# Optimization experiments

Measured on AMD Instinct MI355X. Metric: run time of the kernel, lower is better.

Reference implementation:

```python
import jax, jax.numpy as jnp
import numpy as np
from jax import lax

DN = ('NCHW', 'OIHW', 'NCHW')

def _conv(x, w, b):
    # stride-2 conv, kernel 4, padding 1 (PyTorch Conv2d semantics)
    y = lax.conv_general_dilated(x, w, (2, 2), [(1, 1), (1, 1)], dimension_numbers=DN)
    return y + b[None, :, None, None]

def _deconv(x, w, b):
    # PyTorch ConvTranspose2d(k=4, stride=2, padding=1): conv with lhs_dilation=2,
    # padding k-1-p=2, kernel rot180 with in/out axes swapped ([I,O,H,W] -> [O,I,H,W])
    k = jnp.transpose(jnp.flip(w, (2, 3)), (1, 0, 2, 3))
    y = lax.conv_general_dilated(x, k, (1, 1), [(2, 2), (2, 2)], lhs_dilation=(2, 2),
                                 dimension_numbers=DN)
    return y + b[None, :, None, None]

def setup_inputs() -> dict:
    key = jax.random.key(0)
    ks = jax.random.split(key, 16)
    K, D = 1024, 2048
    s = lambda *sh: 0.05
    inp = {
        'x': jax.random.uniform(ks[0], (8, 3, 256, 256), jnp.float32),
        'enc_w1': jax.random.normal(ks[1], (128, 3, 4, 4), jnp.float32) * 0.05,
        'enc_b1': jnp.zeros((128,), jnp.float32),
        'enc_w2': jax.random.normal(ks[2], (128, 128, 4, 4), jnp.float32) * 0.02,
        'enc_b2': jnp.zeros((128,), jnp.float32),
        'enc_w3': jax.random.normal(ks[3], (D, 128, 4, 4), jnp.float32) * 0.02,
        'enc_b3': jnp.zeros((D,), jnp.float32),
        'codebook': jax.random.uniform(ks[4], (K, D), jnp.float32, -1.0 / K, 1.0 / K),
        'dec_w1': jax.random.normal(ks[5], (D, 128, 4, 4), jnp.float32) * 0.02,  # [in,out,kH,kW]
        'dec_b1': jnp.zeros((128,), jnp.float32),
        'dec_w2': jax.random.normal(ks[6], (128, 128, 4, 4), jnp.float32) * 0.02,
        'dec_b2': jnp.zeros((128,), jnp.float32),
        'dec_w3': jax.random.normal(ks[7], (128, 1, 4, 4), jnp.float32) * 0.05,
        'dec_b3': jnp.zeros((1,), jnp.float32),
    }
    return inp

def reference(x, enc_w1, enc_b1, enc_w2, enc_b2, enc_w3, enc_b3, codebook,
              dec_w1, dec_b1, dec_w2, dec_b2, dec_w3, dec_b3):
    # encoder
    h = jax.nn.relu(_conv(x, enc_w1, enc_b1))
    h = jax.nn.relu(_conv(h, enc_w2, enc_b2))
    z_e = _conv(h, enc_w3, enc_b3)                       # [B, D, H8, W8]
    B, D, Hq, Wq = z_e.shape
    z_flat = z_e.reshape(B, D, Hq * Wq).transpose(0, 2, 1)  # [B, N, D]
    # squared distances to codebook [K, D]
    dists = (jnp.sum(z_flat ** 2, axis=2, keepdims=True)
             + jnp.sum(codebook ** 2, axis=1)
             - 2.0 * jnp.einsum('bnd,kd->bnk', z_flat, codebook))  # [B, N, K]
    idx = jnp.argmin(dists, axis=2)                      # [B, N]
    z_q = codebook[idx]                                  # [B, N, D]
    z_q = z_q.transpose(0, 2, 1).reshape(B, D, Hq, Wq)
    # decoder
    h = jax.nn.relu(_deconv(z_q, dec_w1, dec_b1))
    h = jax.nn.relu(_deconv(h, dec_w2, dec_b2))
    x_recon = jax.nn.sigmoid(_deconv(h, dec_w3, dec_b3))  # [B, 1, H, W]
    sg = lax.stop_gradient
    commitment = 0.25 * jnp.mean((sg(z_e) - z_q) ** 2)
    quantization = jnp.mean((z_e - sg(z_q)) ** 2)
    return x_recon, commitment + quantization
```

## Files before the change

### kernel.cpp

```cpp
#include <hip/hip_runtime.h>

typedef __attribute__((ext_vector_type(8))) short bf16x8;
typedef __attribute__((ext_vector_type(4))) float f32x4;

__device__ __forceinline__ unsigned short f2bf(float f) {
  unsigned u = __float_as_uint(f);
  u += 0x7fff + ((u >> 16) & 1);
  return (unsigned short)(u >> 16);
}
__device__ __forceinline__ float bf2f(unsigned short h) {
  return __uint_as_float(((unsigned)h) << 16);
}

__device__ __forceinline__ void gload_lds16(const void* g, void* l) {
  __builtin_amdgcn_global_load_lds((const __attribute__((address_space(1))) void*)g,
                                   (__attribute__((address_space(3))) void*)l, 16, 0, 0);
}

__device__ __forceinline__ void pbar() {
  asm volatile("" ::: "memory");
  __builtin_amdgcn_sched_barrier(0);
  __builtin_amdgcn_s_barrier();
  __builtin_amdgcn_sched_barrier(0);
  asm volatile("" ::: "memory");
}

__global__ __launch_bounds__(256) void halo_k(unsigned short* __restrict__ h1,
                                              unsigned short* __restrict__ h2,
                                              unsigned short* __restrict__ h3,
                                              unsigned short* __restrict__ h4) {
  int pid = blockIdx.x * 2 + (threadIdx.x >> 7);
  int co = threadIdx.x & 127;
  unsigned short* buf;
  int b, e, SP;
  if (pid < 8256) {
    buf = (pid < 4128) ? h1 : h4;
    int rel = (pid < 4128) ? pid : pid - 4128;
    b = rel / 516; e = rel % 516; SP = 130;
    int y, x;
    if (e < 130) { y = 0; x = e; }
    else if (e < 260) { y = 129; x = e - 130; }
    else if (e < 388) { y = 1 + (e - 260); x = 0; }
    else { y = 1 + (e - 388); x = 129; }
    buf[(((size_t)(b * SP + y)) * SP + x) * 128 + co] = 0;
  } else {
    buf = (pid < 10336) ? h2 : h3;
    int rel = pid - ((pid < 10336) ? 8256 : 10336);
    b = rel / 260; e = rel % 260; SP = 66;
    int y, x;
    if (e < 66) { y = 0; x = e; }
    else if (e < 132) { y = 65; x = e - 66; }
    else if (e < 196) { y = 1 + (e - 132); x = 0; }
    else { y = 1 + (e - 196); x = 65; }
    buf[(((size_t)(b * SP + y)) * SP + x) * 128 + co] = 0;
  }
}

__global__ __launch_bounds__(256) void megapack_k(
    const float* __restrict__ ew2, const float* __restrict__ ew3,
    const float* __restrict__ dw1, const float* __restrict__ dw2,
    const float* __restrict__ dw3, unsigned short* __restrict__ bt2,
    unsigned short* __restrict__ bt3, unsigned short* __restrict__ btw1,
    unsigned short* __restrict__ btd2, float* __restrict__ wd3) {
  int i = blockIdx.x * 256 + threadIdx.x;
  if (i < 262144) {
    int ci = i & 127, kk = (i >> 7) & 15, co = i >> 11;
    bt2[i] = f2bf(ew2[(size_t)co * 2048 + ci * 16 + kk]);
  } else if (i < 4456448) {
    int j = i - 262144;
    int ci = j & 127, kk = (j >> 7) & 15, co = j >> 11;
    bt3[j] = f2bf(ew3[(size_t)co * 2048 + ci * 16 + kk]);
  } else if (i < 8650752) {
    int j = i - 4456448;
    int ci = j & 2047, n = j >> 11;
    int co = n & 127, t = n >> 7;
    btw1[j] = f2bf(dw1[(((size_t)ci * 128 + co) << 4) + t]);
  } else if (i < 8912896) {
    int j = i - 8650752;
    int ci = j & 127, t = (j >> 7) & 3, co = (j >> 9) & 127, z = j >> 16;
    int py = z >> 1, px = z & 1, ty = t >> 1, tx = t & 1;
    int ky = 2 * ty + 1 - py, kx = 2 * tx + 1 - px;
    btd2[j] = f2bf(dw2[(((size_t)ci * 128 + co) * 4 + ky) * 4 + kx]);
  } else {
    int j = i - 8912896;
    int ci = j & 127, t = (j >> 7) & 3, z = j >> 9;
    int py = z >> 1, px = z & 1, ty = t >> 1, tx = t & 1;
    int ky = 2 * ty + 1 - py, kx = 2 * tx + 1 - px;
    wd3[j] = dw3[ci * 16 + ky * 4 + kx];
  }
}

__global__ __launch_bounds__(256) void pack_cb(const float* __restrict__ cb,
                                               unsigned short* __restrict__ cbb,
                                               float* __restrict__ cnorm) {
  int r = blockIdx.x;
  const float* src = cb + (size_t)r * 2048;
  float s = 0.f;
  for (int i = threadIdx.x; i < 2048; i += 256) {
    float v = src[i];
    cbb[(size_t)r * 2048 + i] = f2bf(v);
    s += v * v;
  }
  __shared__ float red[4];
  for (int off = 32; off > 0; off >>= 1) s += __shfl_down(s, off, 64);
  int lane = threadIdx.x & 63, wid = threadIdx.x >> 6;
  if (lane == 0) red[wid] = s;
  __syncthreads();
  if (threadIdx.x == 0) cnorm[r] = red[0] + red[1] + red[2] + red[3];
}

__global__ __launch_bounds__(256) void conv1_k(const float* __restrict__ x,
                                               const float* __restrict__ w1,
                                               const float* __restrict__ b1,
                                               unsigned short* __restrict__ h1) {
  __shared__ float sIn[3][4][258];
  int b = blockIdx.x >> 7, y = blockIdx.x & 127;
  for (int i = threadIdx.x; i < 3 * 4 * 258; i += 256) {
    int c = i / (4 * 258);
    int rr = (i / 258) % 4;
    int col = i % 258;
    int iy = 2 * y - 1 + rr;
    int ix = col - 1;
    float v = (iy >= 0 && iy < 256 && ix >= 0 && ix < 256)
                  ? x[((size_t)(b * 3 + c) * 256 + iy) * 256 + ix] : 0.f;
    sIn[c][rr][col] = v;
  }
  __syncthreads();
  int co = threadIdx.x & 127, xh = threadIdx.x >> 7;
  float w[3][4][4];
#pragma unroll
  for (int c = 0; c < 3; ++c)
#pragma unroll
    for (int ky = 0; ky < 4; ++ky)
#pragma unroll
      for (int kx = 0; kx < 4; ++kx)
        w[c][ky][kx] = w1[(((size_t)co * 3 + c) * 4 + ky) * 4 + kx];
  float bb = b1[co];
  for (int xi = 0; xi < 64; ++xi) {
    int xx = xh * 64 + xi;
    float acc = bb;
#pragma unroll
    for (int c = 0; c < 3; ++c)
#pragma unroll
      for (int ky = 0; ky < 4; ++ky)
#pragma unroll
        for (int kx = 0; kx < 4; ++kx)
          acc += sIn[c][ky][2 * xx + kx] * w[c][ky][kx];
    acc = acc > 0.f ? acc : 0.f;
    h1[((size_t)(b * 130 + y + 1) * 130 + (xx + 1)) * 128 + co] = f2bf(acc);
  }
}

#define GM_CONV 0
#define GM_DECONV 1
#define GM_FLAT 2
#define EP_PM 0
#define EP_FLATBF 1
#define EP_F32 2

struct GP {
  const unsigned short* A;
  const unsigned short* Bt;
  const float* bias;
  void* out;
  int Klen, Clog;
  int MXlog, MYlog;
  int WPin, strideBA;
  int HPo, WPo;
  int Nout;
  int BrowStride;
  int BclassStride;
  int classLog;
  int TPC;
  int outZ;
};

template <int BM, int GM, int EP, int RELU>
__global__ __launch_bounds__(256) void gemm_k(GP p) {
  constexpr int MFR = BM / 32;
  constexpr int CA = BM / 32;
  const int tid = threadIdx.x;
  const int lane = tid & 63;
  const int wid = tid >> 6;
  const int m0 = blockIdx.x * BM;
  const int n0 = blockIdx.y * 128;
  const int zAll = blockIdx.z;
  const int zc = zAll & ((1 << p.classLog) - 1);
  const int chunk = zAll >> p.classLog;
  const int py = zc >> 1, px = zc & 1;

  __shared__ __align__(16) unsigned short sA[BM * 64];
  __shared__ __align__(16) unsigned short sB[128 * 64];

  const unsigned short* Bt = p.Bt + (size_t)zc * p.BclassStride;
  const int C = 1 << p.Clog;
  const int tb = chunk * p.TPC;
  const int chunkOff = tb << p.Clog;
  const int sw = ((lane & 7) ^ (lane >> 3)) * 8;

  int rcA[CA];
#pragma unroll
  for (int i = 0; i < CA; ++i) {
    int r = (wid * CA + i) * 8 + (lane >> 3);
    int m = m0 + r;
    if (GM == GM_FLAT) {
      rcA[i] = m * p.Klen;
    } else {
      int mx = m & ((1 << p.MXlog) - 1);
      int my = (m >> p.MXlog) & ((1 << p.MYlog) - 1);
      int b = m >> (p.MXlog + p.MYlog);
      if (GM == GM_CONV)
        rcA[i] = b * p.strideBA + ((2 * my) * p.WPin + 2 * mx) * C;
      else
        rcA[i] = b * p.strideBA + ((my + 1) * p.WPin + (mx + 1)) * C;
    }
  }
  int rcB[4];
#pragma unroll
  for (int i = 0; i < 4; ++i) {
    int r = (wid * 4 + i) * 8 + (lane >> 3);
    rcB[i] = (n0 + r) * p.BrowStride;
  }

  f32x4 acc[MFR][4];
#pragma unroll
  for (int a = 0; a < MFR; ++a)
#pragma unroll
    for (int b = 0; b < 4; ++b) acc[a][b] = (f32x4){0.f, 0.f, 0.f, 0.f};

  const int nsteps = p.Klen >> 6;
  for (int ks = 0; ks < nsteps; ++ks) {
    const int k0 = ks << 6;
    int tap = 0;
    if (GM == GM_CONV) {
      int t = tb + (k0 >> p.Clog);
      tap = ((t >> 2) * p.WPin + (t & 3)) * C;
    } else if (GM == GM_DECONV) {
      int t = tb + (k0 >> p.Clog);
      int ty = t >> 1, tx = t & 1;
      tap = ((py - ty) * p.WPin + (px - tx)) * C;
    }
    const int ci0 = k0 & (C - 1);
    const int aoff = tap + ci0 + sw;
#pragma unroll
    for (int i = 0; i < CA; ++i)
      gload_lds16(p.A + rcA[i] + aoff, &sA[(wid * CA + i) * 512]);
#pragma unroll
    for (int i = 0; i < 4; ++i)
      gload_lds16(Bt + rcB[i] + chunkOff + k0 + sw, &sB[(wid * 4 + i) * 512]);
    __syncthreads();

#pragma unroll
    for (int kk = 0; kk < 2; ++kk) {
      bf16x8 af[MFR], bfv[4];
#pragma unroll
      for (int mf = 0; mf < MFR; ++mf) {
        int row = (wid >> 1) * (BM / 2) + mf * 16 + (lane & 15);
        int col = (kk * 64 + ((lane >> 4) << 4)) ^ ((row & 7) << 4);
        af[mf] = *(const bf16x8*)((const char*)sA + row * 128 + col);
      }
#pragma unroll
      for (int nf = 0; nf < 4; ++nf) {
        int row = (wid & 1) * 64 + nf * 16 + (lane & 15);
        int col = (kk * 64 + ((lane >> 4) << 4)) ^ ((row & 7) << 4);
        bfv[nf] = *(const bf16x8*)((const char*)sB + row * 128 + col);
      }
#pragma unroll
      for (int mf = 0; mf < MFR; ++mf)
#pragma unroll
        for (int nf = 0; nf < 4; ++nf)
          acc[mf][nf] = __builtin_amdgcn_mfma_f32_16x16x32_bf16(
              af[mf], bfv[nf], acc[mf][nf], 0, 0, 0);
    }
    __syncthreads();
  }

  const int wr = wid >> 1, wc = wid & 1;
#pragma unroll
  for (int mf = 0; mf < MFR; ++mf) {
#pragma unroll
    for (int j = 0; j < 4; ++j) {
      int row = m0 + wr * (BM / 2) + mf * 16 + ((lane >> 4) << 2) + j;
      int b = 0, my = 0, mx = 0;
      if (EP == EP_PM) {
        mx = row & ((1 << p.MXlog) - 1);
        my = (row >> p.MXlog) & ((1 << p.MYlog) - 1);
        b = row >> (p.MXlog + p.MYlog);
      }
#pragma unroll
      for (int nf = 0; nf < 4; ++nf) {
        int col = n0 + wc * 64 + nf * 16 + (lane & 15);
        float v = acc[mf][nf][j];
        if (EP == EP_PM || EP == EP_FLATBF) v += p.bias[col];
        if (RELU) v = v > 0.f ? v : 0.f;
        if (EP == EP_F32) {
          ((float*)p.out)[(size_t)row * p.Nout + col] = v;
        } else if (EP == EP_FLATBF) {
          ((unsigned short*)p.out)[(size_t)row * p.Nout + col] = f2bf(v);
        } else {
          int oy, ox;
          if (GM == GM_DECONV) {
            oy = 2 * my + py + 1;
            ox = 2 * mx + px + 1;
          } else {
            oy = my + 1;
            ox = mx + 1;
          }
          ((unsigned short*)p.out)[((size_t)(b * p.HPo + oy) * p.WPo + ox) * 128 + col] =
              f2bf(v);
        }
      }
    }
  }
}

struct G2 {
  const unsigned short* A;
  const unsigned short* Bt;
  const float* bias;
  unsigned short* out;
  int Klen;
  int WPin, strideBA;
  int Nout;
};

template <int GM>
__global__ __launch_bounds__(512, 2) void gemm256_k(G2 p) {
  __shared__ __align__(16) unsigned short lds[8 * 8192];
  const int tid = threadIdx.x, lane = tid & 63, wid = tid >> 6;
  const int wr = wid >> 2, wc = wid & 3;
  const int m0 = blockIdx.x * 256, n0 = blockIdx.y * 256;
  const int sw = ((lane & 7) ^ (lane >> 3)) * 8;
  const int xc0 = ((lane >> 4) ^ (lane & 7)) * 16;
  const int xc1 = (((lane >> 4) | 4) ^ (lane & 7)) * 16;

  int rcA[2][2], rcB[2][2];
#pragma unroll
  for (int h = 0; h < 2; ++h)
#pragma unroll
    for (int i = 0; i < 2; ++i) {
      int m = m0 + h * 128 + wid * 16 + i * 8 + (lane >> 3);
      if (GM == GM_CONV) {
        int mx = m & 31, my = (m >> 5) & 31, b = m >> 10;
        rcA[h][i] = b * p.strideBA + ((2 * my) * p.WPin + 2 * mx) * 128;
      } else {
        rcA[h][i] = m * p.Klen;
      }
      int n = n0 + h * 128 + wid * 16 + i * 8 + (lane >> 3);
      rcB[h][i] = n * p.Klen;
    }

  const int JMAX = p.Klen >> 4;

  auto stage = [&](int j) {
    if (j >= JMAX) return;
    const int T = j >> 2, type = j & 3, slot = j & 7;
    unsigned short* dst = &lds[slot * 8192 + wid * 1024];
    if (type < 2) {
      const int ko = (T << 6) + sw;
      gload_lds16(p.Bt + rcB[type][0] + ko, dst);
      gload_lds16(p.Bt + rcB[type][1] + ko, dst + 512);
    } else {
      int ko;
      if (GM == GM_CONV) {
        const int t = T >> 1;
        ko = ((t >> 2) * p.WPin + (t & 3)) * 128 + ((T & 1) << 6) + sw;
      } else {
        ko = (T << 6) + sw;
      }
      gload_lds16(p.A + rcA[type - 2][0] + ko, dst);
      gload_lds16(p.A + rcA[type - 2][1] + ko, dst + 512);
    }
  };

  f32x4 acc[8][4];
#pragma unroll
  for (int i = 0; i < 8; ++i)
#pragma unroll
    for (int j = 0; j < 4; ++j) acc[i][j] = (f32x4){0.f, 0.f, 0.f, 0.f};

#pragma unroll
  for (int j = 0; j < 7; ++j) stage(j);
  asm volatile("s_waitcnt vmcnt(6)" ::: "memory");
  pbar();

  const int NT = p.Klen >> 6;
  bf16x8 a[4][2], b0[2][2], b1[2][2];
  for (int t = 0; t < NT; ++t) {
    const int sb = (t & 1) << 2;
    const char* myA = (const char*)&lds[(sb + 2 + wr) * 8192];
    const char* myB = (const char*)&lds[(sb + (wc >> 1)) * 8192];
    const int p4 = t << 2;
#pragma unroll
    for (int mf = 0; mf < 4; ++mf) {
      const int r = mf * 16 + (lane & 15);
      a[mf][0] = *(const bf16x8*)(myA + r * 128 + xc0);
      a[mf][1] = *(const bf16x8*)(myA + r * 128 + xc1);
    }
#pragma unroll
    for (int nf = 0; nf < 2; ++nf) {
      const int c = (wc & 1) * 64 + nf * 16 + (lane & 15);
      b0[nf][0] = *(const bf16x8*)(myB + c * 128 + xc0);
      b0[nf][1] = *(const bf16x8*)(myB + c * 128 + xc1);
    }
    stage(p4 + 7);
    pbar();
    __builtin_amdgcn_s_setprio(1);
#pragma unroll
    for (int mf = 0; mf < 4; ++mf)
#pragma unroll
      for (int nf = 0; nf < 2; ++nf)
#pragma unroll
        for (int kk = 0; kk < 2; ++kk)
          acc[mf][nf] = __builtin_amdgcn_mfma_f32_16x16x32_bf16(
              a[mf][kk], b0[nf][kk], acc[mf][nf], 0, 0, 0);
    __builtin_amdgcn_s_setprio(0);
    pbar();
#pragma unroll
    for (int nf = 0; nf < 2; ++nf) {
      const int c = (wc & 1) * 64 + (nf + 2) * 16 + (lane & 15);
      b1[nf][0] = *(const bf16x8*)(myB + c * 128 + xc0);
      b1[nf][1] = *(const bf16x8*)(myB + c * 128 + xc1);
    }
    stage(p4 + 8);
    pbar();
    __builtin_amdgcn_s_setprio(1);
#pragma unroll
    for (int mf = 0; mf < 4; ++mf)
#pragma unroll
      for (int nf = 0; nf < 2; ++nf)
#pragma unroll
        for (int kk = 0; kk < 2; ++kk)
          acc[mf][nf + 2] = __builtin_amdgcn_mfma_f32_16x16x32_bf16(
              a[mf][kk], b1[nf][kk], acc[mf][nf + 2], 0, 0, 0);
    __builtin_amdgcn_s_setprio(0);
    pbar();
#pragma unroll
    for (int mf = 0; mf < 4; ++mf) {
      const int r = 64 + mf * 16 + (lane & 15);
      a[mf][0] = *(const bf16x8*)(myA + r * 128 + xc0);
      a[mf][1] = *(const bf16x8*)(myA + r * 128 + xc1);
    }
    stage(p4 + 9);
    pbar();
    __builtin_amdgcn_s_setprio(1);
#pragma unroll
    for (int mf = 0; mf < 4; ++mf)
#pragma unroll
      for (int nf = 0; nf < 2; ++nf)
#pragma unroll
        for (int kk = 0; kk < 2; ++kk)
          acc[mf + 4][nf + 2] = __builtin_amdgcn_mfma_f32_16x16x32_bf16(
              a[mf][kk], b1[nf][kk], acc[mf + 4][nf + 2], 0, 0, 0);
    __builtin_amdgcn_s_setprio(0);
    pbar();
    stage(p4 + 10);
    pbar();
    __builtin_amdgcn_s_setprio(1);
#pragma unroll
    for (int mf = 0; mf < 4; ++mf)
#pragma unroll
      for (int nf = 0; nf < 2; ++nf)
#pragma unroll
        for (int kk = 0; kk < 2; ++kk)
          acc[mf + 4][nf] = __builtin_amdgcn_mfma_f32_16x16x32_bf16(
              a[mf][kk], b0[nf][kk], acc[mf + 4][nf], 0, 0, 0);
    __builtin_amdgcn_s_setprio(0);
    asm volatile("s_waitcnt vmcnt(6)" ::: "memory");
    pbar();
  }

#pragma unroll
  for (int mf = 0; mf < 8; ++mf) {
#pragma unroll
    for (int j = 0; j < 4; ++j) {
      int row = m0 + wr * 128 + mf * 16 + ((lane >> 4) << 2) + j;
#pragma unroll
      for (int nf = 0; nf < 4; ++nf) {
        int col = n0 + wc * 64 + nf * 16 + (lane & 15);
        float v = acc[mf][nf][j] + p.bias[col];
        p.out[(size_t)row * p.Nout + col] = f2bf(v);
      }
    }
  }
}

struct GV {
  const unsigned short* A;
  const unsigned short* Bt;
  const float* cnorm;
  float* cval;
  int* cidx;
};

__global__ __launch_bounds__(512, 2) void vq8_k(GV p) {
  __shared__ __align__(16) unsigned short lds[49152];
  const int tid = threadIdx.x, lane = tid & 63, wid = tid >> 6;
  const int wr = wid >> 2, wc = wid & 3;
  const int m0 = blockIdx.x * 128, n0 = blockIdx.y * 256;
  const int sw = ((lane & 7) ^ (lane >> 3)) * 8;
  const int xc0 = ((lane >> 4) ^ (lane & 7)) * 16;
  const int xc1 = (((lane >> 4) | 4) ^ (lane & 7)) * 16;
  const int K = 2048;

  int rcA[2];
#pragma unroll
  for (int h = 0; h < 2; ++h)
    rcA[h] = (m0 + h * 64 + wid * 8 + (lane >> 3)) * K;
  int rcB[2][2];
#pragma unroll
  for (int h = 0; h < 2; ++h)
#pragma unroll
    for (int i = 0; i < 2; ++i)
      rcB[h][i] = (n0 + h * 128 + wid * 16 + i * 8 + (lane >> 3)) * K;

  auto stage = [&](int j) {
    if (j >= 128) return;
    const int T = j >> 2, type = j & 3;
    unsigned short* reg = &lds[(T & 1) * 24576];
    const int ko = (T << 6) + sw;
    if (type < 2) {
      gload_lds16(p.A + rcA[type] + ko, reg + type * 4096 + wid * 512);
    } else {
      unsigned short* d = reg + 8192 + (type - 2) * 8192 + wid * 1024;
      gload_lds16(p.Bt + rcB[type - 2][0] + ko, d);
      gload_lds16(p.Bt + rcB[type - 2][1] + ko, d + 512);
    }
  };

  f32x4 acc[4][4];
#pragma unroll
  for (int i = 0; i < 4; ++i)
#pragma unroll
    for (int j = 0; j < 4; ++j) acc[i][j] = (f32x4){0.f, 0.f, 0.f, 0.f};

#pragma unroll
  for (int j = 0; j < 6; ++j) stage(j);
  asm volatile("s_waitcnt vmcnt(2)" ::: "memory");
  pbar();

  bf16x8 a[4][2], b[4][2];
  for (int t = 0; t < 32; ++t) {
    const char* reg = (const char*)&lds[(t & 1) * 24576];
    const char* myA = reg + wr * 8192;
    const char* myB = reg + 16384 + (wc >> 1) * 16384;
    const int p4 = t << 2;
#pragma unroll
    for (int mf = 0; mf < 4; ++mf) {
      const int r = mf * 16 + (lane & 15);
      a[mf][0] = *(const bf16x8*)(myA + r * 128 + xc0);
      a[mf][1] = *(const bf16x8*)(myA + r * 128 + xc1);
    }
#pragma unroll
    for (int nf = 0; nf < 4; ++nf) {
      const int c = (wc & 1) * 64 + nf * 16 + (lane & 15);
      b[nf][0] = *(const bf16x8*)(myB + c * 128 + xc0);
      b[nf][1] = *(const bf16x8*)(myB + c * 128 + xc1);
    }
    stage(p4 + 6);
    stage(p4 + 7);
    pbar();
    __builtin_amdgcn_s_setprio(1);
#pragma unroll
    for (int mf = 0; mf < 4; ++mf)
#pragma unroll
      for (int nf = 0; nf < 2; ++nf)
#pragma unroll
        for (int kk = 0; kk < 2; ++kk)
          acc[mf][nf] = __builtin_amdgcn_mfma_f32_16x16x32_bf16(
              a[mf][kk], b[nf][kk], acc[mf][nf], 0, 0, 0);
    __builtin_amdgcn_s_setprio(0);
    pbar();
    stage(p4 + 8);
    stage(p4 + 9);
    pbar();
    __builtin_amdgcn_s_setprio(1);
#pragma unroll
    for (int mf = 0; mf < 4; ++mf)
#pragma unroll
      for (int nf = 2; nf < 4; ++nf)
#pragma unroll
        for (int kk = 0; kk < 2; ++kk)
          acc[mf][nf] = __builtin_amdgcn_mfma_f32_16x16x32_bf16(
              a[mf][kk], b[nf][kk], acc[mf][nf], 0, 0, 0);
    __builtin_amdgcn_s_setprio(0);
    asm volatile("s_waitcnt vmcnt(2)" ::: "memory");
    pbar();
  }

  __syncthreads();
  float* sV = (float*)lds;
  int* sI = (int*)(sV + 512);
  float cn[4];
#pragma unroll
  for (int nf = 0; nf < 4; ++nf)
    cn[nf] = p.cnorm[n0 + wc * 64 + nf * 16 + (lane & 15)];
#pragma unroll
  for (int mf = 0; mf < 4; ++mf) {
#pragma unroll
    for (int j = 0; j < 4; ++j) {
      float bv = 3.4e38f;
      int bi = 0x7fffffff;
#pragma unroll
      for (int nf = 0; nf < 4; ++nf) {
        int col = n0 + wc * 64 + nf * 16 + (lane & 15);
        float d = cn[nf] - 2.f * acc[mf][nf][j];
        if (d < bv) { bv = d; bi = col; }
      }
#pragma unroll
      for (int w = 1; w <= 8; w <<= 1) {
        float ov = __shfl_xor(bv, w, 64);
        int oi = __shfl_xor(bi, w, 64);
        if (ov < bv || (ov == bv && oi < bi)) { bv = ov; bi = oi; }
      }
      int lrow = wr * 64 + mf * 16 + ((lane >> 4) << 2) + j;
      if ((lane & 15) == 0) { sV[lrow * 4 + wc] = bv; sI[lrow * 4 + wc] = bi; }
    }
  }
  __syncthreads();
  if (tid < 128) {
    float bv = sV[tid * 4];
    int bi = sI[tid * 4];
#pragma unroll
    for (int c = 1; c < 4; ++c) {
      float v = sV[tid * 4 + c];
      int i2 = sI[tid * 4 + c];
      if (v < bv) { bv = v; bi = i2; }
    }
    p.cval[(size_t)(m0 + tid) * 4 + blockIdx.y] = bv;
    p.cidx[(size_t)(m0 + tid) * 4 + blockIdx.y] = bi;
  }
}

__global__ __launch_bounds__(256) void lossz2_k(const unsigned short* __restrict__ zf,
                                                const float* __restrict__ cval,
                                                const int* __restrict__ cidx,
                                                int* __restrict__ idx,
                                                float* __restrict__ part) {
  int m = blockIdx.x;
  int tid = threadIdx.x;
  bf16x8 av = ((const bf16x8*)(zf + (size_t)m * 2048))[tid];
  float s = 0.f;
#pragma unroll
  for (int i = 0; i < 8; ++i) {
    float z = bf2f((unsigned short)av[i]);
    s += z * z;
  }
  __shared__ float red[4];
  for (int off = 32; off > 0; off >>= 1) s += __shfl_down(s, off, 64);
  int lane = tid & 63, wid = tid >> 6;
  if (lane == 0) red[wid] = s;
  __syncthreads();
  if (tid == 0) {
    float bv = cval[(size_t)m * 4];
    int bi = cidx[(size_t)m * 4];
#pragma unroll
    for (int j = 1; j < 4; ++j) {
      float v = cval[(size_t)m * 4 + j];
      int i2 = cidx[(size_t)m * 4 + j];
      if (v < bv) { bv = v; bi = i2; }
    }
    idx[m] = bi;
    part[m] = red[0] + red[1] + red[2] + red[3] + bv;
  }
}

__global__ __launch_bounds__(256) void loss_final_k(const float* __restrict__ part,
                                                    float* __restrict__ out) {
  int tid = threadIdx.x;
  float s = 0.f;
  for (int i = tid; i < 8192; i += 256) s += part[i];
  __shared__ float red[4];
  for (int off = 32; off > 0; off >>= 1) s += __shfl_down(s, off, 64);
  if ((tid & 63) == 0) red[tid >> 6] = s;
  __syncthreads();
  if (tid == 0) out[0] = 1.25f * (red[0] + red[1] + red[2] + red[3]) / 16777216.f;
}

__global__ __launch_bounds__(256) void dc1gather_k(const float* __restrict__ V,
                                                   const int* __restrict__ idx,
                                                   const float* __restrict__ bias,
                                                   unsigned short* __restrict__ h3) {
  int b = blockIdx.x >> 6;
  int oy = blockIdx.x & 63;
  int co = threadIdx.x & 127;
  int xh = threadIdx.x >> 7;
  __shared__ int sIdx[2][32];
  int iyA = (oy + 1) >> 1, kyA = (oy + 1) & 1;
  int iyB = iyA - 1, kyB = kyA + 2;
  if (threadIdx.x < 64) {
    int which = threadIdx.x >> 5;
    int ix = threadIdx.x & 31;
    int iy = which ? iyB : iyA;
    sIdx[which][ix] = (iy >= 0 && iy < 32) ? idx[(b << 10) + (iy << 5) + ix] : -1;
  }
  __syncthreads();
  float bb = bias[co];
  for (int xi = 0; xi < 32; ++xi) {
    int ox = xh * 32 + xi;
    int ixA = (ox + 1) >> 1, kxA = (ox + 1) & 1;
    int ixB = ixA - 1, kxB = kxA + 2;
    float s = bb;
    int kAA = (ixA < 32) ? sIdx[0][ixA] : -1;
    if (kAA >= 0) s += V[((size_t)(kAA * 16 + kyA * 4 + kxA)) * 128 + co];
    int kAB = (ixB >= 0) ? sIdx[0][ixB] : -1;
    if (kAB >= 0) s += V[((size_t)(kAB * 16 + kyA * 4 + kxB)) * 128 + co];
    int kBA = (ixA < 32) ? sIdx[1][ixA] : -1;
    if (kBA >= 0) s += V[((size_t)(kBA * 16 + kyB * 4 + kxA)) * 128 + co];
    int kBB = (ixB >= 0) ? sIdx[1][ixB] : -1;
    if (kBB >= 0) s += V[((size_t)(kBB * 16 + kyB * 4 + kxB)) * 128 + co];
    s = s > 0.f ? s : 0.f;
    h3[((size_t)(b * 66 + oy + 1) * 66 + (ox + 1)) * 128 + co] = f2bf(s);
  }
}

__global__ __launch_bounds__(256) void deconv3_k(const unsigned short* __restrict__ h4,
                                                 const float* __restrict__ wd,
                                                 const float* __restrict__ b3,
                                                 float* __restrict__ out) {
  __shared__ __align__(16) char sRow[2 * 130 * 272];
  __shared__ float sW[2048];
  const int tid = threadIdx.x;
  const int b = blockIdx.x >> 8, oy = blockIdx.x & 255;
  const int py = oy & 1, uy = oy >> 1;
  const int g0 = uy + py;
  for (int i = tid; i < 2048; i += 256) sW[i] = wd[i];
  for (int g = tid; g < 4160; g += 256) {
    int r = (g >= 2080) ? 1 : 0;
    int gg = g - r * 2080;
    int px = gg >> 4, k = gg & 15;
    const bf16x8* src =
        (const bf16x8*)(h4 + (((size_t)(b * 130 + g0 + r) * 130 + px) << 7) + k * 8);
    *(bf16x8*)(sRow + r * 35360 + px * 272 + k * 16) = *src;
  }
  __syncthreads();
  const int ox = tid;
  const int pxp = ox & 1, ux = ox >> 1;
  const int z = py * 2 + pxp;
  float s = b3[0];
#pragma unroll
  for (int ty = 0; ty < 2; ++ty) {
#pragma unroll
    for (int tx = 0; tx < 2; ++tx) {
      int ixp = ux + 1 + pxp - tx;
      const char* base = sRow + (1 - ty) * 35360 + ixp * 272;
      const float* wp = &sW[z * 512 + (ty * 2 + tx) * 128];
#pragma unroll
      for (int k = 0; k < 16; ++k) {
        bf16x8 v = *(const bf16x8*)(base + k * 16);
#pragma unroll
        for (int i = 0; i < 8; ++i)
          s += bf2f((unsigned short)v[i]) * wp[k * 8 + i];
      }
    }
  }
  out[(size_t)blockIdx.x * 256 + ox] = 1.f / (1.f + __expf(-s));
}

extern "C" void kernel_launch(void* const* d_in, const int* in_sizes, int n_in,
                              void* d_out, int out_size, void* d_ws, size_t ws_size,
                              hipStream_t stream) {
  const float* x = (const float*)d_in[0];
  const float* ew1 = (const float*)d_in[1];
  const float* eb1 = (const float*)d_in[2];
  const float* ew2 = (const float*)d_in[3];
  const float* eb2 = (const float*)d_in[4];
  const float* ew3 = (const float*)d_in[5];
  const float* eb3 = (const float*)d_in[6];
  const float* cb = (const float*)d_in[7];
  const float* dw1 = (const float*)d_in[8];
  const float* db1 = (const float*)d_in[9];
  const float* dw2 = (const float*)d_in[10];
  const float* db2 = (const float*)d_in[11];
  const float* dw3 = (const float*)d_in[12];
  const float* db3 = (const float*)d_in[13];
  float* out = (float*)d_out;

  char* w = (char*)d_ws;
  size_t off = 0;
  auto alloc = [&](size_t bytes) {
    char* p = w + off;
    off = (off + bytes + 255) & ~(size_t)255;
    return p;
  };
  const size_t sz_h1 = 8ull * 130 * 130 * 128 * 2;
  const size_t sz_h2 = 8ull * 66 * 66 * 128 * 2;
  const size_t sz_zf = 8192ull * 2048 * 2;
  unsigned short* h1 = (unsigned short*)alloc(sz_h1);
  unsigned short* h2 = (unsigned short*)alloc(sz_h2);
  unsigned short* zf = (unsigned short*)alloc(sz_zf);
  unsigned short* cbb = (unsigned short*)alloc(1024ull * 2048 * 2);
  float* cnorm = (float*)alloc(1024 * 4);
  int* idx = (int*)alloc(8192 * 4);
  unsigned short* h4 = (unsigned short*)alloc(sz_h1);
  unsigned short* bt2 = (unsigned short*)alloc(128ull * 2048 * 2);
  unsigned short* bt3 = (unsigned short*)alloc(2048ull * 2048 * 2);
  unsigned short* btw1 = (unsigned short*)alloc(2048ull * 2048 * 2);
  unsigned short* btd2 = (unsigned short*)alloc(4ull * 128 * 512 * 2);
  float* V = (float*)alloc(1024ull * 16 * 128 * 4);
  float* lpart = (float*)alloc(8192 * 4);
  float* wd3 = (float*)alloc(2048 * 4);
  unsigned short* h3 = (unsigned short*)alloc(sz_h2);
  float* cval = (float*)alloc(8192ull * 4 * 4);
  int* cidx = (int*)alloc(8192ull * 4 * 4);

  halo_k<<<6208, 256, 0, stream>>>(h1, h2, h3, h4);
  megapack_k<<<34824, 256, 0, stream>>>(ew2, ew3, dw1, dw2, dw3,
                                        bt2, bt3, btw1, btd2, wd3);
  pack_cb<<<1024, 256, 0, stream>>>(cb, cbb, cnorm);
  conv1_k<<<1024, 256, 0, stream>>>(x, ew1, eb1, h1);

  GP pcw = {cbb, btw1, nullptr, V, 2048, 11, 0, 0, 0, 0, 0, 0,
            2048, 2048, 0, 0, 0, 0};
  gemm_k<64, GM_FLAT, EP_F32, 0><<<dim3(16, 16, 1), 256, 0, stream>>>(pcw);

  GP p2 = {h1, bt2, eb2, h2, 2048, 7, 6, 6, 130, 130 * 130 * 128, 66, 66,
           128, 2048, 0, 0, 0, 0};
  gemm_k<64, GM_CONV, EP_PM, 1><<<dim3(512, 1, 1), 256, 0, stream>>>(p2);

  G2 g3 = {h2, bt3, eb3, zf, 2048, 66, 66 * 66 * 128, 2048};
  gemm256_k<GM_CONV><<<dim3(32, 8, 1), 512, 0, stream>>>(g3);

  GV pv = {zf, cbb, cnorm, cval, cidx};
  vq8_k<<<dim3(64, 4, 1), 512, 0, stream>>>(pv);

  lossz2_k<<<8192, 256, 0, stream>>>(zf, cval, cidx, idx, lpart);
  loss_final_k<<<1, 256, 0, stream>>>(lpart, out + 524288);

  dc1gather_k<<<512, 256, 0, stream>>>(V, idx, db1, h3);

  GP pd2 = {h3, btd2, db2, h4, 512, 7, 6, 6, 66, 66 * 66 * 128, 130, 130,
            128, 512, 128 * 512, 2, 0, 0};
  gemm_k<128, GM_DECONV, EP_PM, 1><<<dim3(256, 1, 4), 256, 0, stream>>>(pd2);

  deconv3_k<<<2048, 256, 0, stream>>>(h4, wd3, db3, out);
  (void)in_sizes; (void)n_in; (void)out_size; (void)ws_size;
}
```

Measured before the change: 386.7 us.

## Merge preamble kernels into one launch and halve GEMM loop phases

Measured after the change: 383.9 us. About the same (-0.7%).

```diff
diff --git a/kernel.cpp b/kernel.cpp
--- a/kernel.cpp
+++ b/kernel.cpp
@@ -25,129 +25,125 @@
   asm volatile("" ::: "memory");
 }
 
-__global__ __launch_bounds__(256) void halo_k(unsigned short* __restrict__ h1,
-                                              unsigned short* __restrict__ h2,
-                                              unsigned short* __restrict__ h3,
-                                              unsigned short* __restrict__ h4) {
-  int pid = blockIdx.x * 2 + (threadIdx.x >> 7);
-  int co = threadIdx.x & 127;
-  unsigned short* buf;
-  int b, e, SP;
-  if (pid < 8256) {
-    buf = (pid < 4128) ? h1 : h4;
-    int rel = (pid < 4128) ? pid : pid - 4128;
-    b = rel / 516; e = rel % 516; SP = 130;
-    int y, x;
-    if (e < 130) { y = 0; x = e; }
-    else if (e < 260) { y = 129; x = e - 130; }
-    else if (e < 388) { y = 1 + (e - 260); x = 0; }
-    else { y = 1 + (e - 388); x = 129; }
-    buf[(((size_t)(b * SP + y)) * SP + x) * 128 + co] = 0;
+__global__ __launch_bounds__(256) void preamble_k(
+    const float* __restrict__ x, const float* __restrict__ ew1,
+    const float* __restrict__ eb1, const float* __restrict__ ew2,
+    const float* __restrict__ ew3, const float* __restrict__ dw1,
+    const float* __restrict__ dw2, const float* __restrict__ dw3,
+    const float* __restrict__ cb, unsigned short* __restrict__ h1,
+    unsigned short* __restrict__ h2, unsigned short* __restrict__ h3,
+    unsigned short* __restrict__ h4, unsigned short* __restrict__ bt2,
+    unsigned short* __restrict__ bt3, unsigned short* __restrict__ btw1,
+    unsigned short* __restrict__ btd2, float* __restrict__ wd3,
+    unsigned short* __restrict__ cbb, float* __restrict__ cnorm) {
+  __shared__ float sIn[3][4][258];
+  __shared__ float red[4];
+  const int blk = blockIdx.x;
+  const int tid = threadIdx.x;
+  if (blk < 6208) {
+    int pid = blk * 2 + (tid >> 7);
+    int co = tid & 127;
+    unsigned short* buf;
+    int b, e, SP;
+    if (pid < 8256) {
+      buf = (pid < 4128) ? h1 : h4;
+      int rel = (pid < 4128) ? pid : pid - 4128;
+      b = rel / 516; e = rel % 516; SP = 130;
+      int y, xx;
+      if (e < 130) { y = 0; xx = e; }
+      else if (e < 260) { y = 129; xx = e - 130; }
+      else if (e < 388) { y = 1 + (e - 260); xx = 0; }
+      else { y = 1 + (e - 388); xx = 129; }
+      buf[(((size_t)(b * SP + y)) * SP + xx) * 128 + co] = 0;
+    } else {
+      buf = (pid < 10336) ? h2 : h3;
+      int rel = pid - ((pid < 10336) ? 8256 : 10336);
+      b = rel / 260; e = rel % 260; SP = 66;
+      int y, xx;
+      if (e < 66) { y = 0; xx = e; }
+      else if (e < 132) { y = 65; xx = e - 66; }
+      else if (e < 196) { y = 1 + (e - 132); xx = 0; }
+      else { y = 1 + (e - 196); xx = 65; }
+      buf[(((size_t)(b * SP + y)) * SP + xx) * 128 + co] = 0;
+    }
+  } else if (blk < 41032) {
+    int i = (blk - 6208) * 256 + tid;
+    if (i < 262144) {
+      int ci = i & 127, kk = (i >> 7) & 15, co = i >> 11;
+      bt2[i] = f2bf(ew2[(size_t)co * 2048 + ci * 16 + kk]);
+    } else if (i < 4456448) {
+      int j = i - 262144;
+      int ci = j & 127, kk = (j >> 7) & 15, co = j >> 11;
+      bt3[j] = f2bf(ew3[(size_t)co * 2048 + ci * 16 + kk]);
+    } else if (i < 8650752) {
+      int j = i - 4456448;
+      int ci = j & 2047, n = j >> 11;
+      int co = n & 127, t = n >> 7;
+      btw1[j] = f2bf(dw1[(((size_t)ci * 128 + co) << 4) + t]);
+    } else if (i < 8912896) {
+      int j = i - 8650752;
+      int ci = j & 127, t = (j >> 7) & 3, co = (j >> 9) & 127, z = j >> 16;
+      int py = z >> 1, px = z & 1, ty = t >> 1, tx = t & 1;
+      int ky = 2 * ty + 1 - py, kx = 2 * tx + 1 - px;
+      btd2[j] = f2bf(dw2[(((size_t)ci * 128 + co) * 4 + ky) * 4 + kx]);
+    } else {
+      int j = i - 8912896;
+      int ci = j & 127, t = (j >> 7) & 3, z = j >> 9;
+      int py = z >> 1, px = z & 1, ty = t >> 1, tx = t & 1;
+      int ky = 2 * ty + 1 - py, kx = 2 * tx + 1 - px;
+      wd3[j] = dw3[ci * 16 + ky * 4 + kx];
+    }
+  } else if (blk < 42056) {
+    int r = blk - 41032;
+    const float* src = cb + (size_t)r * 2048;
+    float s = 0.f;
+    for (int i = tid; i < 2048; i += 256) {
+      float v = src[i];
+      cbb[(size_t)r * 2048 + i] = f2bf(v);
+      s += v * v;
+    }
+    for (int off2 = 32; off2 > 0; off2 >>= 1) s += __shfl_down(s, off2, 64);
+    int lane = tid & 63, wid = tid >> 6;
+    if (lane == 0) red[wid] = s;
+    __syncthreads();
+    if (tid == 0) cnorm[r] = red[0] + red[1] + red[2] + red[3];
   } else {
-    buf = (pid < 10336) ? h2 : h3;
-    int rel = pid - ((pid < 10336) ? 8256 : 10336);
-    b = rel / 260; e = rel % 260; SP = 66;
-    int y, x;
-    if (e < 66) { y = 0; x = e; }
-    else if (e < 132) { y = 65; x = e - 66; }
-    else if (e < 196) { y = 1 + (e - 132); x = 0; }
-    else { y = 1 + (e - 196); x = 65; }
-    buf[(((size_t)(b * SP + y)) * SP + x) * 128 + co] = 0;
-  }
-}
-
-__global__ __launch_bounds__(256) void megapack_k(
-    const float* __restrict__ ew2, const float* __restrict__ ew3,
-    const float* __restrict__ dw1, const float* __restrict__ dw2,
-    const float* __restrict__ dw3, unsigned short* __restrict__ bt2,
-    unsigned short* __restrict__ bt3, unsigned short* __restrict__ btw1,
-    unsigned short* __restrict__ btd2, float* __restrict__ wd3) {
-  int i = blockIdx.x * 256 + threadIdx.x;
-  if (i < 262144) {
-    int ci = i & 127, kk = (i >> 7) & 15, co = i >> 11;
-    bt2[i] = f2bf(ew2[(size_t)co * 2048 + ci * 16 + kk]);
-  } else if (i < 4456448) {
-    int j = i - 262144;
-    int ci = j & 127, kk = (j >> 7) & 15, co = j >> 11;
-    bt3[j] = f2bf(ew3[(size_t)co * 2048 + ci * 16 + kk]);
-  } else if (i < 8650752) {
-    int j = i - 4456448;
-    int ci = j & 2047, n = j >> 11;
-    int co = n & 127, t = n >> 7;
-    btw1[j] = f2bf(dw1[(((size_t)ci * 128 + co) << 4) + t]);
-  } else if (i < 8912896) {
-    int j = i - 8650752;
-    int ci = j & 127, t = (j >> 7) & 3, co = (j >> 9) & 127, z = j >> 16;
-    int py = z >> 1, px = z & 1, ty = t >> 1, tx = t & 1;
-    int ky = 2 * ty + 1 - py, kx = 2 * tx + 1 - px;
-    btd2[j] = f2bf(dw2[(((size_t)ci * 128 + co) * 4 + ky) * 4 + kx]);
-  } else {
-    int j = i - 8912896;
-    int ci = j & 127, t = (j >> 7) & 3, z = j >> 9;
-    int py = z >> 1, px = z & 1, ty = t >> 1, tx = t & 1;
-    int ky = 2 * ty + 1 - py, kx = 2 * tx + 1 - px;
-    wd3[j] = dw3[ci * 16 + ky * 4 + kx];
-  }
-}
-
-__global__ __launch_bounds__(256) void pack_cb(const float* __restrict__ cb,
-                                               unsigned short* __restrict__ cbb,
-                                               float* __restrict__ cnorm) {
-  int r = blockIdx.x;
-  const float* src = cb + (size_t)r * 2048;
-  float s = 0.f;
-  for (int i = threadIdx.x; i < 2048; i += 256) {
-    float v = src[i];
-    cbb[(size_t)r * 2048 + i] = f2bf(v);
-    s += v * v;
-  }
-  __shared__ float red[4];
-  for (int off = 32; off > 0; off >>= 1) s += __shfl_down(s, off, 64);
-  int lane = threadIdx.x & 63, wid = threadIdx.x >> 6;
-  if (lane == 0) red[wid] = s;
-  __syncthreads();
-  if (threadIdx.x == 0) cnorm[r] = red[0] + red[1] + red[2] + red[3];
-}
-
-__global__ __launch_bounds__(256) void conv1_k(const float* __restrict__ x,
-                                               const float* __restrict__ w1,
-                                               const float* __restrict__ b1,
-                                               unsigned short* __restrict__ h1) {
-  __shared__ float sIn[3][4][258];
-  int b = blockIdx.x >> 7, y = blockIdx.x & 127;
-  for (int i = threadIdx.x; i < 3 * 4 * 258; i += 256) {
-    int c = i / (4 * 258);
-    int rr = (i / 258) % 4;
-    int col = i % 258;
-    int iy = 2 * y - 1 + rr;
-    int ix = col - 1;
-    float v = (iy >= 0 && iy < 256 && ix >= 0 && ix < 256)
-                  ? x[((size_t)(b * 3 + c) * 256 + iy) * 256 + ix] : 0.f;
-    sIn[c][rr][col] = v;
-  }
-  __syncthreads();
-  int co = threadIdx.x & 127, xh = threadIdx.x >> 7;
-  float w[3][4][4];
-#pragma unroll
-  for (int c = 0; c < 3; ++c)
-#pragma unroll
-    for (int ky = 0; ky < 4; ++ky)
-#pragma unroll
-      for (int kx = 0; kx < 4; ++kx)
-        w[c][ky][kx] = w1[(((size_t)co * 3 + c) * 4 + ky) * 4 + kx];
-  float bb = b1[co];
-  for (int xi = 0; xi < 64; ++xi) {
-    int xx = xh * 64 + xi;
-    float acc = bb;
+    int rel = blk - 42056;
+    int b = rel >> 7, y = rel & 127;
+    for (int i = tid; i < 3 * 4 * 258; i += 256) {
+      int c = i / (4 * 258);
+      int rr = (i / 258) % 4;
+      int col = i % 258;
+      int iy = 2 * y - 1 + rr;
+      int ix = col - 1;
+      float v = (iy >= 0 && iy < 256 && ix >= 0 && ix < 256)
+                    ? x[((size_t)(b * 3 + c) * 256 + iy) * 256 + ix] : 0.f;
+      sIn[c][rr][col] = v;
+    }
+    __syncthreads();
+    int co = tid & 127, xh = tid >> 7;
+    float w[3][4][4];
 #pragma unroll
     for (int c = 0; c < 3; ++c)
 #pragma unroll
       for (int ky = 0; ky < 4; ++ky)
 #pragma unroll
         for (int kx = 0; kx < 4; ++kx)
-          acc += sIn[c][ky][2 * xx + kx] * w[c][ky][kx];
-    acc = acc > 0.f ? acc : 0.f;
-    h1[((size_t)(b * 130 + y + 1) * 130 + (xx + 1)) * 128 + co] = f2bf(acc);
+          w[c][ky][kx] = ew1[(((size_t)co * 3 + c) * 4 + ky) * 4 + kx];
+    float bb = eb1[co];
+    for (int xi = 0; xi < 64; ++xi) {
+      int xx = xh * 64 + xi;
+      float acc = bb;
+#pragma unroll
+      for (int c = 0; c < 3; ++c)
+#pragma unroll
+        for (int ky = 0; ky < 4; ++ky)
+#pragma unroll
+          for (int kx = 0; kx < 4; ++kx)
+            acc += sIn[c][ky][2 * xx + kx] * w[c][ky][kx];
+      acc = acc > 0.f ? acc : 0.f;
+      h1[((size_t)(b * 130 + y + 1) * 130 + (xx + 1)) * 128 + co] = f2bf(acc);
+    }
   }
 }
 
@@ -380,12 +376,12 @@
     for (int j = 0; j < 4; ++j) acc[i][j] = (f32x4){0.f, 0.f, 0.f, 0.f};
 
 #pragma unroll
-  for (int j = 0; j < 7; ++j) stage(j);
-  asm volatile("s_waitcnt vmcnt(6)" ::: "memory");
+  for (int j = 0; j < 6; ++j) stage(j);
+  asm volatile("s_waitcnt vmcnt(4)" ::: "memory");
   pbar();
 
   const int NT = p.Klen >> 6;
-  bf16x8 a[4][2], b0[2][2], b1[2][2];
+  bf16x8 a[4][2], b[4][2];
   for (int t = 0; t < NT; ++t) {
     const int sb = (t & 1) << 2;
     const char* myA = (const char*)&lds[(sb + 2 + wr) * 8192];
@@ -398,41 +394,23 @@
       a[mf][1] = *(const bf16x8*)(myA + r * 128 + xc1);
     }
 #pragma unroll
-    for (int nf = 0; nf < 2; ++nf) {
+    for (int nf = 0; nf < 4; ++nf) {
       const int c = (wc & 1) * 64 + nf * 16 + (lane & 15);
-      b0[nf][0] = *(const bf16x8*)(myB + c * 128 + xc0);
-      b0[nf][1] = *(const bf16x8*)(myB + c * 128 + xc1);
-    }
+      b[nf][0] = *(const bf16x8*)(myB + c * 128 + xc0);
+      b[nf][1] = *(const bf16x8*)(myB + c * 128 + xc1);
+    }
+    stage(p4 + 6);
     stage(p4 + 7);
     pbar();
     __builtin_amdgcn_s_setprio(1);
 #pragma unroll
     for (int mf = 0; mf < 4; ++mf)
 #pragma unroll
-      for (int nf = 0; nf < 2; ++nf)
+      for (int nf = 0; nf < 4; ++nf)
 #pragma unroll
         for (int kk = 0; kk < 2; ++kk)
           acc[mf][nf] = __builtin_amdgcn_mfma_f32_16x16x32_bf16(
-              a[mf][kk], b0[nf][kk], acc[mf][nf], 0, 0, 0);
-    __builtin_amdgcn_s_setprio(0);
-    pbar();
-#pragma unroll
-    for (int nf = 0; nf < 2; ++nf) {
-      const int c = (wc & 1) * 64 + (nf + 2) * 16 + (lane & 15);
-      b1[nf][0] = *(const bf16x8*)(myB + c * 128 + xc0);
-      b1[nf][1] = *(const bf16x8*)(myB + c * 128 + xc1);
-    }
-    stage(p4 + 8);
-    pbar();
-    __builtin_amdgcn_s_setprio(1);
-#pragma unroll
-    for (int mf = 0; mf < 4; ++mf)
-#pragma unroll
-      for (int nf = 0; nf < 2; ++nf)
-#pragma unroll
-        for (int kk = 0; kk < 2; ++kk)
-          acc[mf][nf + 2] = __builtin_amdgcn_mfma_f32_16x16x32_bf16(
-              a[mf][kk], b1[nf][kk], acc[mf][nf + 2], 0, 0, 0);
+              a[mf][kk], b[nf][kk], acc[mf][nf], 0, 0, 0);
     __builtin_amdgcn_s_setprio(0);
     pbar();
 #pragma unroll
@@ -441,32 +419,20 @@
       a[mf][0] = *(const bf16x8*)(myA + r * 128 + xc0);
       a[mf][1] = *(const bf16x8*)(myA + r * 128 + xc1);
     }
+    stage(p4 + 8);
     stage(p4 + 9);
     pbar();
     __builtin_amdgcn_s_setprio(1);
 #pragma unroll
     for (int mf = 0; mf < 4; ++mf)
 #pragma unroll
-      for (int nf = 0; nf < 2; ++nf)
-#pragma unroll
-        for (int kk = 0; kk < 2; ++kk)
-          acc[mf + 4][nf + 2] = __builtin_amdgcn_mfma_f32_16x16x32_bf16(
-              a[mf][kk], b1[nf][kk], acc[mf + 4][nf + 2], 0, 0, 0);
-    __builtin_amdgcn_s_setprio(0);
-    pbar();
-    stage(p4 + 10);
-    pbar();
-    __builtin_amdgcn_s_setprio(1);
-#pragma unroll
-    for (int mf = 0; mf < 4; ++mf)
-#pragma unroll
-      for (int nf = 0; nf < 2; ++nf)
+      for (int nf = 0; nf < 4; ++nf)
 #pragma unroll
         for (int kk = 0; kk < 2; ++kk)
           acc[mf + 4][nf] = __builtin_amdgcn_mfma_f32_16x16x32_bf16(
-              a[mf][kk], b0[nf][kk], acc[mf + 4][nf], 0, 0, 0);
+              a[mf][kk], b[nf][kk], acc[mf + 4][nf], 0, 0, 0);
     __builtin_amdgcn_s_setprio(0);
-    asm volatile("s_waitcnt vmcnt(6)" ::: "memory");
+    asm volatile("s_waitcnt vmcnt(4)" ::: "memory");
     pbar();
   }
 
@@ -804,11 +770,9 @@
   float* cval = (float*)alloc(8192ull * 4 * 4);
   int* cidx = (int*)alloc(8192ull * 4 * 4);
 
-  halo_k<<<6208, 256, 0, stream>>>(h1, h2, h3, h4);
-  megapack_k<<<34824, 256, 0, stream>>>(ew2, ew3, dw1, dw2, dw3,
-                                        bt2, bt3, btw1, btd2, wd3);
-  pack_cb<<<1024, 256, 0, stream>>>(cb, cbb, cnorm);
-  conv1_k<<<1024, 256, 0, stream>>>(x, ew1, eb1, h1);
+  preamble_k<<<43080, 256, 0, stream>>>(x, ew1, eb1, ew2, ew3, dw1, dw2, dw3, cb,
+                                        h1, h2, h3, h4, bt2, bt3, btw1, btd2,
+                                        wd3, cbb, cnorm);
 
   GP pcw = {cbb, btw1, nullptr, V, 2048, 11, 0, 0, 0, 0, 0, 0,
             2048, 2048, 0, 0, 0, 0};
```
